# Performance work log

Hardware: AMD Instinct MI355X
Metric: run time of the kernel (lower is better)

## Reference

```python
import jax, jax.numpy as jnp
import numpy as np
from math import sqrt

B, T, C, H = 4, 2048, 1024, 16
D = C // H  # head dim = 64


def setup_inputs() -> dict:
    key = jax.random.key(0)
    ks = jax.random.split(key, 9)
    s = 1.0 / sqrt(C)
    return {
        "x": jax.random.normal(ks[0], (B, T, C), dtype=jnp.float32),
        "Wk": jax.random.normal(ks[1], (C, C), dtype=jnp.float32) * s,
        "bk": jax.random.normal(ks[2], (C,), dtype=jnp.float32) * 0.01,
        "Wq": jax.random.normal(ks[3], (C, C), dtype=jnp.float32) * s,
        "bq": jax.random.normal(ks[4], (C,), dtype=jnp.float32) * 0.01,
        "Wv": jax.random.normal(ks[5], (C, C), dtype=jnp.float32) * s,
        "bv": jax.random.normal(ks[6], (C,), dtype=jnp.float32) * 0.01,
        "Wp": jax.random.normal(ks[7], (C, C), dtype=jnp.float32) * s,
        "bp": jax.random.normal(ks[8], (C,), dtype=jnp.float32) * 0.01,
    }


def reference(x, Wk, bk, Wq, bq, Wv, bv, Wp, bp):
    # Linear projections, split into heads: [B, H, T, D]
    def heads(y):
        return y.reshape(B, T, H, D).transpose(0, 2, 1, 3)

    k = heads(x @ Wk + bk)
    q = heads(x @ Wq + bq)
    v = heads(x @ Wv + bv)

    # scaled dot-product attention with causal mask (dropout p=0 -> identity)
    attn = jnp.einsum("bhtd,bhsd->bhts", q, k) / jnp.sqrt(jnp.float32(D))
    causal = jnp.tril(jnp.ones((T, T), dtype=bool))
    attn = jnp.where(causal[None, None], attn, -jnp.inf)
    attn = jax.nn.softmax(attn, axis=-1)

    y = jnp.einsum("bhts,bhsd->bhtd", attn, v)  # [B, H, T, D]
    y = y.transpose(0, 2, 1, 3).reshape(B, T, C)
    return y @ Wp + bp
```

## Files before the change

kernel.cpp:

```cpp
#include <hip/hip_runtime.h>
#include <hip/hip_bf16.h>
#include <math.h>


typedef short bf16x8 __attribute__((ext_vector_type(8)));
typedef float f32x4 __attribute__((ext_vector_type(4)));
typedef _Float16 f16x4 __attribute__((ext_vector_type(4)));

__device__ __forceinline__ short f2b(float f) {
    unsigned u = __float_as_uint(f);
    u = (u + 0x7fffu + ((u >> 16) & 1u)) >> 16;
    return (short)u;
}
__device__ __forceinline__ float b2f(short s) {
    return __uint_as_float(((unsigned)(unsigned short)s) << 16);
}

__global__ __launch_bounds__(256) void cast_x_kernel(const float* __restrict__ x,
                                                     short* __restrict__ xb, int n4) {
    int idx = blockIdx.x * 256 + threadIdx.x;
    if (idx >= n4) return;
    float4 v = ((const float4*)x)[idx];
    short4 o;
    o.x = f2b(v.x); o.y = f2b(v.y); o.z = f2b(v.z); o.w = f2b(v.w);
    ((short4*)xb)[idx] = o;
}

__global__ __launch_bounds__(256) void wtrans_kernel(const float* W0, const float* W1,
                                                     const float* W2, const float* W3,
                                                     short* O0, short* O1, short* O2, short* O3) {
    const float* W; short* O;
    switch (blockIdx.z) {
        case 0: W = W0; O = O0; break;
        case 1: W = W1; O = O1; break;
        case 2: W = W2; O = O2; break;
        default: W = W3; O = O3; break;
    }
    __shared__ __align__(16) float Ls[64 * 68];
    int tid = threadIdx.x;
    int n0 = blockIdx.x * 64, k0 = blockIdx.y * 64;
    #pragma unroll
    for (int it = 0; it < 4; ++it) {
        int c = tid + it * 256;
        int r = c >> 4, off = (c & 15) * 4;
        *(float4*)&Ls[r * 68 + off] = *(const float4*)&W[(k0 + r) * 1024 + n0 + off];
    }
    __syncthreads();
    #pragma unroll
    for (int it = 0; it < 2; ++it) {
        int c = tid + it * 256;
        int n = c >> 3, koff = (c & 7) * 8;
        union { short s[8]; int4 v; } u;
        #pragma unroll
        for (int k = 0; k < 8; ++k) u.s[k] = f2b(Ls[(koff + k) * 68 + n]);
        *(int4*)&O[(n0 + n) * 1024 + k0 + koff] = u.v;
    }
}

template<int MODE>
__global__ __launch_bounds__(256) void gemm_kernel(const short* __restrict__ A,
                                                   const short* Bt0, const short* Bt1, const short* Bt2,
                                                   const float* b0, const float* b1, const float* b2,
                                                   float s0, float s1, float s2,
                                                   void* O0, void* O1, void* O2) {
    int z = blockIdx.z;
    const short* Bt   = (z == 0) ? Bt0 : (z == 1) ? Bt1 : Bt2;
    const float* bias = (z == 0) ? b0  : (z == 1) ? b1  : b2;
    float scl         = (z == 0) ? s0  : (z == 1) ? s1  : s2;
    void* Out         = (z == 0) ? O0  : (z == 1) ? O1  : O2;

    __shared__ __align__(16) short As[128 * 64];
    __shared__ __align__(16) short Bs[128 * 64];

    int tid = threadIdx.x;
    int w = tid >> 6, lane = tid & 63, quad = lane >> 4, l15 = lane & 15;
    int m0 = blockIdx.x * 128, n0 = blockIdx.y * 128;
    int wm = (w >> 1) * 64, wn = (w & 1) * 64;
    int lrow = lane >> 3, lcol = (lane & 7) * 8;

    f32x4 acc[4][4] = {};

    for (int kt = 0; kt < 16; ++kt) {
        int k0 = kt * 64;
        __syncthreads();
        #pragma unroll
        for (int it = 0; it < 4; ++it) {
            int r0 = it * 32 + w * 8;
            __builtin_amdgcn_global_load_lds(
                (const __attribute__((address_space(1))) unsigned int*)&A[(m0 + r0 + lrow) * 1024 + k0 + lcol],
                (__attribute__((address_space(3))) unsigned int*)&As[r0 * 64], 16, 0, 0);
            __builtin_amdgcn_global_load_lds(
                (const __attribute__((address_space(1))) unsigned int*)&Bt[(n0 + r0 + lrow) * 1024 + k0 + lcol],
                (__attribute__((address_space(3))) unsigned int*)&Bs[r0 * 64], 16, 0, 0);
        }
        __syncthreads();
        #pragma unroll
        for (int kk = 0; kk < 2; ++kk) {
            bf16x8 af[4], bf[4];
            #pragma unroll
            for (int i = 0; i < 4; ++i)
                af[i] = *(const bf16x8*)&As[(wm + i * 16 + l15) * 64 + kk * 32 + quad * 8];
            #pragma unroll
            for (int j = 0; j < 4; ++j)
                bf[j] = *(const bf16x8*)&Bs[(wn + j * 16 + l15) * 64 + kk * 32 + quad * 8];
            #pragma unroll
            for (int i = 0; i < 4; ++i)
                #pragma unroll
                for (int j = 0; j < 4; ++j)
                    acc[i][j] = __builtin_amdgcn_mfma_f32_16x16x32_bf16(af[i], bf[j], acc[i][j], 0, 0, 0);
        }
    }
    #pragma unroll
    for (int i = 0; i < 4; ++i) {
        #pragma unroll
        for (int j = 0; j < 4; ++j) {
            int gn = n0 + wn + j * 16 + l15;
            float bv = bias[gn];
            #pragma unroll
            for (int r = 0; r < 4; ++r) {
                int gm = m0 + wm + i * 16 + quad * 4 + r;
                float v = (acc[i][j][r] + bv) * scl;
                if (MODE == 0) {
                    int b = gm >> 11, t = gm & 2047, h = gn >> 6, d = gn & 63;
                    ((short*)Out)[(((b * 16 + h) * 2048) + t) * 64 + d] = f2b(v);
                } else {
                    ((float*)Out)[gm * 1024 + gn] = v;
                }
            }
        }
    }
}

__global__ __launch_bounds__(256) void vtrans_kernel(const short* __restrict__ V,
                                                     _Float16* __restrict__ Vt) {
    __shared__ __align__(16) short Ts[64 * 72];
    int tid = threadIdx.x;
    int bh = blockIdx.y;
    int t0 = blockIdx.x * 64;
    #pragma unroll
    for (int it = 0; it < 2; ++it) {
        int c = tid + it * 256;
        int r = c >> 3, off = (c & 7) * 8;
        *(int4*)&Ts[r * 72 + off] = *(const int4*)&V[(bh * 2048 + t0 + r) * 64 + off];
    }
    __syncthreads();
    #pragma unroll
    for (int it = 0; it < 2; ++it) {
        int c = tid + it * 256;
        int d = c >> 3, toff = (c & 7) * 8;
        union { _Float16 h[8]; int4 v; } u;
        #pragma unroll
        for (int k = 0; k < 8; ++k) u.h[k] = (_Float16)b2f(Ts[(toff + k) * 72 + d]);
        *(int4*)&Vt[(bh * 64 + d) * 2048 + t0 + toff] = u.v;
    }
}

__global__ __launch_bounds__(256, 3) void attn_kernel(const short* __restrict__ Q,
                                                      const short* __restrict__ K,
                                                      const _Float16* __restrict__ Vt,
                                                      short* __restrict__ Y) {
    __shared__ __align__(16) short    Ks[128 * 64];
    __shared__ __align__(16) _Float16 Vs[64 * 128];

    int tid = threadIdx.x;
    int w = tid >> 6, lane = tid & 63, quad = lane >> 4, l15 = lane & 15;
    int idx = blockIdx.x;
    int qi = 15 - (idx >> 6);
    int bh = idx & 63;

    const short* Qh = Q + bh * 2048 * 64;
    const short* Kh = K + bh * 2048 * 64;
    const _Float16* Vh = Vt + bh * 64 * 2048;

    bf16x8 qf[2][2];
    #pragma unroll
    for (int i = 0; i < 2; ++i)
        #pragma unroll
        for (int kh = 0; kh < 2; ++kh) {
            int t = qi * 128 + w * 32 + i * 16 + l15;
            qf[i][kh] = *(const bf16x8*)&Qh[t * 64 + kh * 32 + quad * 8];
        }

    int krow = lane >> 3;
    int kchunk = ((lane & 7) ^ krow) * 8;
    int vrow = lane >> 4;
    int vchunk = ((lane & 15) ^ (w * 4 + vrow)) * 8;

    int t7 = l15 & 7;
    int kf0_off = ((quad ^ t7) * 8);
    int kf1_off = (((quad + 4) ^ t7) * 8);
    int vsub = (quad & 1) * 4;
    int vchi = quad >> 1;

    f32x4 o[2][4] = {};
    float lsum[2] = {0.f, 0.f};

    for (int si = 0; si <= qi; ++si) {
        const short* Kt = Kh + si * 128 * 64;
        const _Float16* Vtile = Vh + si * 128;
        bool diag = (si == qi);

        __syncthreads();
        #pragma unroll
        for (int it = 0; it < 4; ++it) {
            int kr0 = it * 32 + w * 8;
            __builtin_amdgcn_global_load_lds(
                (const __attribute__((address_space(1))) unsigned int*)&Kt[(kr0 + krow) * 64 + kchunk],
                (__attribute__((address_space(3))) unsigned int*)&Ks[kr0 * 64], 16, 0, 0);
            int vr0 = it * 16 + w * 4;
            __builtin_amdgcn_global_load_lds(
                (const __attribute__((address_space(1))) unsigned int*)&Vtile[(vr0 + vrow) * 2048 + vchunk],
                (__attribute__((address_space(3))) unsigned int*)&Vs[vr0 * 128], 16, 0, 0);
        }
        __syncthreads();

        #pragma unroll
        for (int j = 0; j < 8; ++j) {
            int trow = (j * 16 + l15) * 64;
            bf16x8 kf0 = *(const bf16x8*)&Ks[trow + kf0_off];
            bf16x8 kf1 = *(const bf16x8*)&Ks[trow + kf1_off];
            f16x4 pfv[2];
            #pragma unroll
            for (int i = 0; i < 2; ++i) {
                f32x4 a = {};
                a = __builtin_amdgcn_mfma_f32_16x16x32_bf16(kf0, qf[i][0], a, 0, 0, 0);
                a = __builtin_amdgcn_mfma_f32_16x16x32_bf16(kf1, qf[i][1], a, 0, 0, 0);
                if (diag) {
                    int qrel = w * 32 + i * 16 + l15;
                    #pragma unroll
                    for (int r = 0; r < 4; ++r)
                        if (j * 16 + quad * 4 + r > qrel) a[r] = -1e30f;
                }
                float p0 = __builtin_amdgcn_exp2f(a[0]);
                float p1 = __builtin_amdgcn_exp2f(a[1]);
                float p2 = __builtin_amdgcn_exp2f(a[2]);
                float p3 = __builtin_amdgcn_exp2f(a[3]);
                lsum[i] += (p0 + p1) + (p2 + p3);
                pfv[i][0] = (_Float16)p0;
                pfv[i][1] = (_Float16)p1;
                pfv[i][2] = (_Float16)p2;
                pfv[i][3] = (_Float16)p3;
            }
            int vc = (j * 2 + vchi);
            #pragma unroll
            for (int mt = 0; mt < 4; ++mt) {
                int d = mt * 16 + l15;
                f16x4 vf = *(const f16x4*)&Vs[d * 128 + ((vc ^ l15) * 8) + vsub];
                o[0][mt] = __builtin_amdgcn_mfma_f32_16x16x16f16(vf, pfv[0], o[0][mt], 0, 0, 0);
                o[1][mt] = __builtin_amdgcn_mfma_f32_16x16x16f16(vf, pfv[1], o[1][mt], 0, 0, 0);
            }
        }
    }

    int b = bh >> 4, h = bh & 15;
    #pragma unroll
    for (int i = 0; i < 2; ++i) {
        float l = lsum[i];
        l += __shfl_xor(l, 16);
        l += __shfl_xor(l, 32);
        float rinv = 1.0f / l;
        int q = qi * 128 + w * 32 + i * 16 + l15;
        short* yrow = &Y[(b * 2048 + q) * 1024 + h * 64];
        #pragma unroll
        for (int mt = 0; mt < 4; ++mt) {
            short4 s4;
            s4.x = f2b(o[i][mt][0] * rinv);
            s4.y = f2b(o[i][mt][1] * rinv);
            s4.z = f2b(o[i][mt][2] * rinv);
            s4.w = f2b(o[i][mt][3] * rinv);
            *(short4*)&yrow[mt * 16 + quad * 4] = s4;
        }
    }
}

extern "C" void kernel_launch(void* const* d_in, const int* in_sizes, int n_in,
                              void* d_out, int out_size, void* d_ws, size_t ws_size,
                              hipStream_t stream) {
    const float* x  = (const float*)d_in[0];
    const float* Wk = (const float*)d_in[1];
    const float* bk = (const float*)d_in[2];
    const float* Wq = (const float*)d_in[3];
    const float* bq = (const float*)d_in[4];
    const float* Wv = (const float*)d_in[5];
    const float* bv = (const float*)d_in[6];
    const float* Wp = (const float*)d_in[7];
    const float* bp = (const float*)d_in[8];

    char* ws = (char*)d_ws;
    short*     xb  = (short*)(ws + 0);
    short*     Wqt = (short*)(ws + 16777216);
    short*     Wkt = (short*)(ws + 18874368);
    short*     Wvt = (short*)(ws + 20971520);
    short*     Wpt = (short*)(ws + 23068672);
    short*     Qb  = (short*)(ws + 25165824);
    short*     Kb  = (short*)(ws + 41943040);
    short*     Vb  = (short*)(ws + 58720256);
    _Float16*  Vtb = (_Float16*)(ws + 75497472);
    short*     Yb  = (short*)(ws + 92274688);

    cast_x_kernel<<<8192, 256, 0, stream>>>(x, xb, 2097152);
    wtrans_kernel<<<dim3(16, 16, 4), 256, 0, stream>>>(Wq, Wk, Wv, Wp, Wqt, Wkt, Wvt, Wpt);
    gemm_kernel<0><<<dim3(64, 8, 3), 256, 0, stream>>>(xb, Wqt, Wkt, Wvt, bq, bk, bv,
                                                       0.18033688011112042f , 1.0f, 1.0f,
                                                       (void*)Qb, (void*)Kb, (void*)Vb);
    vtrans_kernel<<<dim3(32, 64), 256, 0, stream>>>(Vb, Vtb);
    attn_kernel<<<1024, 256, 0, stream>>>(Qb, Kb, Vtb, Yb);
    gemm_kernel<1><<<dim3(64, 8, 1), 256, 0, stream>>>(Yb, Wpt, nullptr, nullptr,
                                                       bp, nullptr, nullptr,
                                                       1.0f, 1.0f, 1.0f,
                                                       (void*)d_out, nullptr, nullptr);
}
```

Measured before the change: 254.7 us.

## Fuse V transpose into GEMM epilogue, pair causal query tiles, double-buffer K/V

The QKV GEMM epilogue now writes V directly as transposed fp16, which removes the separate vtrans kernel and its extra round trip through memory. The attention kernel now gives each block two query tiles (p and 15-p) so causal work is balanced across blocks, and the grid is halved. Each K/V tile loaded into LDS is shared by both query tiles. K/V loads are double-buffered in LDS so the next tile is fetched while the current one is computed, at the cost of twice the LDS, more registers, and occupancy lowered to 2 blocks per CU.

New measurement: 256.5 us. Within noise of the previous version (+0.7%).

```diff
diff --git a/kernel.cpp b/kernel.cpp
--- a/kernel.cpp
+++ b/kernel.cpp
@@ -11,9 +11,6 @@
     unsigned u = __float_as_uint(f);
     u = (u + 0x7fffu + ((u >> 16) & 1u)) >> 16;
     return (short)u;
-}
-__device__ __forceinline__ float b2f(short s) {
-    return __uint_as_float(((unsigned)(unsigned short)s) << 16);
 }
 
 __global__ __launch_bounds__(256) void cast_x_kernel(const float* __restrict__ x,
@@ -116,158 +113,197 @@
         for (int j = 0; j < 4; ++j) {
             int gn = n0 + wn + j * 16 + l15;
             float bv = bias[gn];
-            #pragma unroll
-            for (int r = 0; r < 4; ++r) {
-                int gm = m0 + wm + i * 16 + quad * 4 + r;
-                float v = (acc[i][j][r] + bv) * scl;
-                if (MODE == 0) {
-                    int b = gm >> 11, t = gm & 2047, h = gn >> 6, d = gn & 63;
-                    ((short*)Out)[(((b * 16 + h) * 2048) + t) * 64 + d] = f2b(v);
-                } else {
-                    ((float*)Out)[gm * 1024 + gn] = v;
+            if (MODE == 0 && z == 2) {
+                int h = gn >> 6, d = gn & 63;
+                int gm0 = m0 + wm + i * 16 + quad * 4;
+                int b = gm0 >> 11, t = gm0 & 2047;
+                f16x4 hv;
+                #pragma unroll
+                for (int r = 0; r < 4; ++r) hv[r] = (_Float16)(acc[i][j][r] + bv);
+                *(f16x4*)&((_Float16*)Out)[(((b * 16 + h) * 64) + d) * 2048 + t] = hv;
+            } else {
+                #pragma unroll
+                for (int r = 0; r < 4; ++r) {
+                    int gm = m0 + wm + i * 16 + quad * 4 + r;
+                    float v = (acc[i][j][r] + bv) * scl;
+                    if (MODE == 0) {
+                        int b = gm >> 11, t = gm & 2047, h = gn >> 6, d = gn & 63;
+                        ((short*)Out)[(((b * 16 + h) * 2048) + t) * 64 + d] = f2b(v);
+                    } else {
+                        ((float*)Out)[gm * 1024 + gn] = v;
+                    }
                 }
             }
         }
     }
 }
 
-__global__ __launch_bounds__(256) void vtrans_kernel(const short* __restrict__ V,
-                                                     _Float16* __restrict__ Vt) {
-    __shared__ __align__(16) short Ts[64 * 72];
-    int tid = threadIdx.x;
-    int bh = blockIdx.y;
-    int t0 = blockIdx.x * 64;
-    #pragma unroll
-    for (int it = 0; it < 2; ++it) {
-        int c = tid + it * 256;
-        int r = c >> 3, off = (c & 7) * 8;
-        *(int4*)&Ts[r * 72 + off] = *(const int4*)&V[(bh * 2048 + t0 + r) * 64 + off];
-    }
-    __syncthreads();
-    #pragma unroll
-    for (int it = 0; it < 2; ++it) {
-        int c = tid + it * 256;
-        int d = c >> 3, toff = (c & 7) * 8;
-        union { _Float16 h[8]; int4 v; } u;
-        #pragma unroll
-        for (int k = 0; k < 8; ++k) u.h[k] = (_Float16)b2f(Ts[(toff + k) * 72 + d]);
-        *(int4*)&Vt[(bh * 64 + d) * 2048 + t0 + toff] = u.v;
-    }
-}
-
-__global__ __launch_bounds__(256, 3) void attn_kernel(const short* __restrict__ Q,
+__global__ __launch_bounds__(256, 2) void attn_kernel(const short* __restrict__ Q,
                                                       const short* __restrict__ K,
                                                       const _Float16* __restrict__ Vt,
                                                       short* __restrict__ Y) {
-    __shared__ __align__(16) short    Ks[128 * 64];
-    __shared__ __align__(16) _Float16 Vs[64 * 128];
+    __shared__ __align__(16) short    Ks[2][128 * 64];
+    __shared__ __align__(16) _Float16 Vs[2][64 * 128];
 
     int tid = threadIdx.x;
     int w = tid >> 6, lane = tid & 63, quad = lane >> 4, l15 = lane & 15;
     int idx = blockIdx.x;
-    int qi = 15 - (idx >> 6);
+    int p = idx >> 6;
     int bh = idx & 63;
+    int qa = p, qb = 15 - p;
 
     const short* Qh = Q + bh * 2048 * 64;
     const short* Kh = K + bh * 2048 * 64;
     const _Float16* Vh = Vt + bh * 64 * 2048;
 
-    bf16x8 qf[2][2];
+    bf16x8 qfa[2][2], qfb[2][2];
     #pragma unroll
     for (int i = 0; i < 2; ++i)
         #pragma unroll
         for (int kh = 0; kh < 2; ++kh) {
-            int t = qi * 128 + w * 32 + i * 16 + l15;
-            qf[i][kh] = *(const bf16x8*)&Qh[t * 64 + kh * 32 + quad * 8];
+            int ra = qa * 128 + w * 32 + i * 16 + l15;
+            int rb = qb * 128 + w * 32 + i * 16 + l15;
+            qfa[i][kh] = *(const bf16x8*)&Qh[ra * 64 + kh * 32 + quad * 8];
+            qfb[i][kh] = *(const bf16x8*)&Qh[rb * 64 + kh * 32 + quad * 8];
         }
 
     int krow = lane >> 3;
     int kchunk = ((lane & 7) ^ krow) * 8;
     int vrow = lane >> 4;
     int vchunk = ((lane & 15) ^ (w * 4 + vrow)) * 8;
-
     int t7 = l15 & 7;
-    int kf0_off = ((quad ^ t7) * 8);
-    int kf1_off = (((quad + 4) ^ t7) * 8);
+    int kf0_off = (quad ^ t7) * 8;
+    int kf1_off = ((quad + 4) ^ t7) * 8;
     int vsub = (quad & 1) * 4;
     int vchi = quad >> 1;
 
-    f32x4 o[2][4] = {};
-    float lsum[2] = {0.f, 0.f};
-
-    for (int si = 0; si <= qi; ++si) {
-        const short* Kt = Kh + si * 128 * 64;
-        const _Float16* Vtile = Vh + si * 128;
-        bool diag = (si == qi);
-
-        __syncthreads();
+    f32x4 oa[2][4] = {}, ob[2][4] = {};
+    float la[2] = {0.f, 0.f}, lb[2] = {0.f, 0.f};
+
+    auto stage = [&](int s, int bsel) {
+        const short* Kt = Kh + s * 128 * 64;
+        const _Float16* Vtile = Vh + s * 128;
+        short* KsD = &Ks[bsel][0];
+        _Float16* VsD = &Vs[bsel][0];
         #pragma unroll
         for (int it = 0; it < 4; ++it) {
             int kr0 = it * 32 + w * 8;
             __builtin_amdgcn_global_load_lds(
                 (const __attribute__((address_space(1))) unsigned int*)&Kt[(kr0 + krow) * 64 + kchunk],
-                (__attribute__((address_space(3))) unsigned int*)&Ks[kr0 * 64], 16, 0, 0);
+                (__attribute__((address_space(3))) unsigned int*)&KsD[kr0 * 64], 16, 0, 0);
             int vr0 = it * 16 + w * 4;
             __builtin_amdgcn_global_load_lds(
                 (const __attribute__((address_space(1))) unsigned int*)&Vtile[(vr0 + vrow) * 2048 + vchunk],
-                (__attribute__((address_space(3))) unsigned int*)&Vs[vr0 * 128], 16, 0, 0);
-        }
-        __syncthreads();
+                (__attribute__((address_space(3))) unsigned int*)&VsD[vr0 * 128], 16, 0, 0);
+        }
+    };
+
+    stage(0, 0);
+    __syncthreads();
+
+    for (int si = 0; si <= qb; ++si) {
+        int buf = si & 1;
+        if (si < qb) stage(si + 1, buf ^ 1);
+
+        const short* KsB = &Ks[buf][0];
+        const _Float16* VsB = &Vs[buf][0];
+        bool do_a = (si <= qa);
+        bool diag_a = (si == qa), diag_b = (si == qb);
 
         #pragma unroll
         for (int j = 0; j < 8; ++j) {
             int trow = (j * 16 + l15) * 64;
-            bf16x8 kf0 = *(const bf16x8*)&Ks[trow + kf0_off];
-            bf16x8 kf1 = *(const bf16x8*)&Ks[trow + kf1_off];
-            f16x4 pfv[2];
+            bf16x8 kf0 = *(const bf16x8*)&KsB[trow + kf0_off];
+            bf16x8 kf1 = *(const bf16x8*)&KsB[trow + kf1_off];
+            int vc = j * 2 + vchi;
+            f16x4 vf[4];
+            #pragma unroll
+            for (int mt = 0; mt < 4; ++mt)
+                vf[mt] = *(const f16x4*)&VsB[(mt * 16 + l15) * 128 + ((vc ^ l15) * 8) + vsub];
+
             #pragma unroll
             for (int i = 0; i < 2; ++i) {
                 f32x4 a = {};
-                a = __builtin_amdgcn_mfma_f32_16x16x32_bf16(kf0, qf[i][0], a, 0, 0, 0);
-                a = __builtin_amdgcn_mfma_f32_16x16x32_bf16(kf1, qf[i][1], a, 0, 0, 0);
-                if (diag) {
+                a = __builtin_amdgcn_mfma_f32_16x16x32_bf16(kf0, qfb[i][0], a, 0, 0, 0);
+                a = __builtin_amdgcn_mfma_f32_16x16x32_bf16(kf1, qfb[i][1], a, 0, 0, 0);
+                if (diag_b) {
                     int qrel = w * 32 + i * 16 + l15;
                     #pragma unroll
                     for (int r = 0; r < 4; ++r)
                         if (j * 16 + quad * 4 + r > qrel) a[r] = -1e30f;
                 }
+                f16x4 pfv;
                 float p0 = __builtin_amdgcn_exp2f(a[0]);
                 float p1 = __builtin_amdgcn_exp2f(a[1]);
                 float p2 = __builtin_amdgcn_exp2f(a[2]);
                 float p3 = __builtin_amdgcn_exp2f(a[3]);
-                lsum[i] += (p0 + p1) + (p2 + p3);
-                pfv[i][0] = (_Float16)p0;
-                pfv[i][1] = (_Float16)p1;
-                pfv[i][2] = (_Float16)p2;
-                pfv[i][3] = (_Float16)p3;
+                lb[i] += (p0 + p1) + (p2 + p3);
+                pfv[0] = (_Float16)p0; pfv[1] = (_Float16)p1;
+                pfv[2] = (_Float16)p2; pfv[3] = (_Float16)p3;
+                #pragma unroll
+                for (int mt = 0; mt < 4; ++mt)
+                    ob[i][mt] = __builtin_amdgcn_mfma_f32_16x16x16f16(vf[mt], pfv, ob[i][mt], 0, 0, 0);
             }
-            int vc = (j * 2 + vchi);
-            #pragma unroll
-            for (int mt = 0; mt < 4; ++mt) {
-                int d = mt * 16 + l15;
-                f16x4 vf = *(const f16x4*)&Vs[d * 128 + ((vc ^ l15) * 8) + vsub];
-                o[0][mt] = __builtin_amdgcn_mfma_f32_16x16x16f16(vf, pfv[0], o[0][mt], 0, 0, 0);
-                o[1][mt] = __builtin_amdgcn_mfma_f32_16x16x16f16(vf, pfv[1], o[1][mt], 0, 0, 0);
+            if (do_a) {
+                #pragma unroll
+                for (int i = 0; i < 2; ++i) {
+                    f32x4 a = {};
+                    a = __builtin_amdgcn_mfma_f32_16x16x32_bf16(kf0, qfa[i][0], a, 0, 0, 0);
+                    a = __builtin_amdgcn_mfma_f32_16x16x32_bf16(kf1, qfa[i][1], a, 0, 0, 0);
+                    if (diag_a) {
+                        int qrel = w * 32 + i * 16 + l15;
+                        #pragma unroll
+                        for (int r = 0; r < 4; ++r)
+                            if (j * 16 + quad * 4 + r > qrel) a[r] = -1e30f;
+                    }
+                    f16x4 pfv;
+                    float p0 = __builtin_amdgcn_exp2f(a[0]);
+                    float p1 = __builtin_amdgcn_exp2f(a[1]);
+                    float p2 = __builtin_amdgcn_exp2f(a[2]);
+                    float p3 = __builtin_amdgcn_exp2f(a[3]);
+                    la[i] += (p0 + p1) + (p2 + p3);
+                    pfv[0] = (_Float16)p0; pfv[1] = (_Float16)p1;
+                    pfv[2] = (_Float16)p2; pfv[3] = (_Float16)p3;
+                    #pragma unroll
+                    for (int mt = 0; mt < 4; ++mt)
+                        oa[i][mt] = __builtin_amdgcn_mfma_f32_16x16x16f16(vf[mt], pfv, oa[i][mt], 0, 0, 0);
+                }
             }
         }
+        __syncthreads();
     }
 
     int b = bh >> 4, h = bh & 15;
     #pragma unroll
     for (int i = 0; i < 2; ++i) {
-        float l = lsum[i];
+        float l = la[i];
         l += __shfl_xor(l, 16);
         l += __shfl_xor(l, 32);
         float rinv = 1.0f / l;
-        int q = qi * 128 + w * 32 + i * 16 + l15;
+        int q = qa * 128 + w * 32 + i * 16 + l15;
         short* yrow = &Y[(b * 2048 + q) * 1024 + h * 64];
         #pragma unroll
         for (int mt = 0; mt < 4; ++mt) {
             short4 s4;
-            s4.x = f2b(o[i][mt][0] * rinv);
-            s4.y = f2b(o[i][mt][1] * rinv);
-            s4.z = f2b(o[i][mt][2] * rinv);
-            s4.w = f2b(o[i][mt][3] * rinv);
+            s4.x = f2b(oa[i][mt][0] * rinv);
+            s4.y = f2b(oa[i][mt][1] * rinv);
+            s4.z = f2b(oa[i][mt][2] * rinv);
+            s4.w = f2b(oa[i][mt][3] * rinv);
+            *(short4*)&yrow[mt * 16 + quad * 4] = s4;
+        }
+        l = lb[i];
+        l += __shfl_xor(l, 16);
+        l += __shfl_xor(l, 32);
+        rinv = 1.0f / l;
+        q = qb * 128 + w * 32 + i * 16 + l15;
+        yrow = &Y[(b * 2048 + q) * 1024 + h * 64];
+        #pragma unroll
+        for (int mt = 0; mt < 4; ++mt) {
+            short4 s4;
+            s4.x = f2b(ob[i][mt][0] * rinv);
+            s4.y = f2b(ob[i][mt][1] * rinv);
+            s4.z = f2b(ob[i][mt][2] * rinv);
+            s4.w = f2b(ob[i][mt][3] * rinv);
             *(short4*)&yrow[mt * 16 + quad * 4] = s4;
         }
     }
@@ -294,7 +330,6 @@
     short*     Wpt = (short*)(ws + 23068672);
     short*     Qb  = (short*)(ws + 25165824);
     short*     Kb  = (short*)(ws + 41943040);
-    short*     Vb  = (short*)(ws + 58720256);
     _Float16*  Vtb = (_Float16*)(ws + 75497472);
     short*     Yb  = (short*)(ws + 92274688);
 
@@ -302,9 +337,8 @@
     wtrans_kernel<<<dim3(16, 16, 4), 256, 0, stream>>>(Wq, Wk, Wv, Wp, Wqt, Wkt, Wvt, Wpt);
     gemm_kernel<0><<<dim3(64, 8, 3), 256, 0, stream>>>(xb, Wqt, Wkt, Wvt, bq, bk, bv,
                                                        0.18033688011112042f , 1.0f, 1.0f,
-                                                       (void*)Qb, (void*)Kb, (void*)Vb);
-    vtrans_kernel<<<dim3(32, 64), 256, 0, stream>>>(Vb, Vtb);
-    attn_kernel<<<1024, 256, 0, stream>>>(Qb, Kb, Vtb, Yb);
+                                                       (void*)Qb, (void*)Kb, (void*)Vtb);
+    attn_kernel<<<512, 256, 0, stream>>>(Qb, Kb, Vtb, Yb);
     gemm_kernel<1><<<dim3(64, 8, 1), 256, 0, stream>>>(Yb, Wpt, nullptr, nullptr,
                                                        bp, nullptr, nullptr,
                                                        1.0f, 1.0f, 1.0f,
```
